# Kernel tuning notes

Measured on AMD Instinct MI355X. Metric: run time of the kernel, lower is better.

## Reference

```python
import jax, jax.numpy as jnp
import numpy as np

NEG_SLOPE = 0.2  # PyG GATConv default negative_slope
EPS = 1e-16      # PyG softmax denominator epsilon


def setup_inputs() -> dict:
    key = jax.random.key(0)
    N, C, H, E = 50000, 64, 12, 400000
    k = jax.random.split(key, 5)
    x = jax.random.normal(k[0], (N, C), dtype=jnp.float32)
    edge_index = jax.random.randint(k[1], (2, E), 0, N, dtype=jnp.int32)
    W = jax.random.normal(k[2], (C, H * C), dtype=jnp.float32) * (1.0 / np.sqrt(C))
    att_src = jax.random.normal(k[3], (H, C), dtype=jnp.float32) * 0.1
    att_dst = jax.random.normal(k[4], (H, C), dtype=jnp.float32) * 0.1
    bias = jnp.zeros((C,), dtype=jnp.float32)
    return {"x": x, "edge_index": edge_index, "W": W,
            "att_src": att_src, "att_dst": att_dst, "bias": bias}


def reference(x, edge_index, W, att_src, att_dst, bias):
    N, C = x.shape
    H = att_src.shape[0]
    # GATConv default add_self_loops=True
    loops = jnp.arange(N, dtype=edge_index.dtype)
    src = jnp.concatenate([edge_index[0], loops])  # message source j
    dst = jnp.concatenate([edge_index[1], loops])  # message target i

    h = (x @ W).reshape(N, H, C)                   # [N,H,C] projected features
    a_src = jnp.einsum('nhc,hc->nh', h, att_src)   # [N,H]
    a_dst = jnp.einsum('nhc,hc->nh', h, att_dst)   # [N,H]

    alpha = jax.nn.leaky_relu(a_src[src] + a_dst[dst], NEG_SLOPE)  # [E',H]
    # segment softmax over destination neighborhoods
    m = jax.ops.segment_max(alpha, dst, num_segments=N)
    alpha = jnp.exp(alpha - m[dst])
    denom = jax.ops.segment_sum(alpha, dst, num_segments=N)
    alpha = alpha / (denom[dst] + EPS)

    msg = h[src] * alpha[:, :, None]               # [E',H,C]
    out = jax.ops.segment_sum(msg, dst, num_segments=N)  # [N,H,C]
    y = out.mean(axis=1) + bias                    # concat=False -> head mean
    return jax.nn.relu(x + y)
```

## Files before the change

### kernel.cpp

```cpp
#include <hip/hip_runtime.h>
#include <hip/hip_bf16.h>


typedef __bf16 bf16x8 __attribute__((ext_vector_type(8)));
typedef float  f32x4  __attribute__((ext_vector_type(4)));
typedef float  f32x2  __attribute__((ext_vector_type(2)));

#define HEADS 12
#define CH 64
#define HC 768
#define CAP 64
#define ACOLS 24
#define ZSTRIDE 776

__device__ inline float readlane_f(float v, int lane) {
    return __builtin_bit_cast(float,
        __builtin_amdgcn_readlane(__builtin_bit_cast(int, v), lane));
}

__global__ __launch_bounds__(256) void k_pre(
    const float* __restrict__ W,
    const float* __restrict__ att_src, const float* __restrict__ att_dst,
    int* __restrict__ cnt, __bf16* __restrict__ Wt2, __bf16* __restrict__ Vt,
    int N) {
    const int nb_z = (N + 255) >> 8;
    const int nb_w = (CH * HC) >> 8;
    int b = blockIdx.x, tid = threadIdx.x;
    if (b < nb_z) {
        int i = b * 256 + tid;
        if (i < N) cnt[i] = 0;
        return;
    }
    b -= nb_z;
    if (b < nb_w) {
        int t = b * 256 + tid;
        int c = t / HC, kk = t % HC;
        int k = kk & 63;
        Wt2[t] = (__bf16)W[(size_t)k * HC + (kk - k) + c];
        return;
    }
    b -= nb_w;
    if (b >= 2 * HEADS) {
        if (tid < CH) Vt[b * CH + tid] = (__bf16)0.f;
        return;
    }
    const float* att = (b < HEADS) ? att_src + b * CH
                                   : att_dst + (b - HEADS) * CH;
    int k = tid >> 2, cq = tid & 3;
    const float* wr = W + (size_t)k * HC + (b % HEADS) * CH + cq * 16;
    float s = 0.f;
#pragma unroll
    for (int j = 0; j < 16; ++j) s += wr[j] * att[cq * 16 + j];
    s += __shfl_xor(s, 1, 64);
    s += __shfl_xor(s, 2, 64);
    if (cq == 0) Vt[b * CH + k] = (__bf16)s;
}

__global__ __launch_bounds__(256) void k_main(
    const float* __restrict__ x, const int* __restrict__ ei,
    const __bf16* __restrict__ Vt,
    int* __restrict__ cnt, int* __restrict__ adj,
    __bf16* __restrict__ xb, float* __restrict__ a_all, int N, int E) {
    const int EP = E + N;
    const int nb_build = (EP + 255) >> 8;
    int b = blockIdx.x, tid = threadIdx.x;

    if (b < nb_build) {
        int e = b * 256 + tid;
        if (e < EP) {
            int d, s;
            if (e < E) { d = ei[E + e]; s = ei[e]; }
            else       { d = e - E;     s = d; }
            int pos = atomicAdd(&cnt[d], 1);
            if (pos < CAP) adj[d * CAP + pos] = s;
        }
        return;
    }
    b -= nb_build;
    int wave = tid >> 6, lane = tid & 63;
    int m = lane & 15, quad = lane >> 4;
    int m0 = b * 64 + wave * 16;
    int row = m0 + m;
    int rc = row < N ? row : N - 1;
    const float* xa = x + (size_t)rc * CH + quad * 8;
    f32x4 v0 = *(const f32x4*)xa;
    f32x4 v1 = *(const f32x4*)(xa + 4);
    f32x4 v2 = *(const f32x4*)(xa + 32);
    f32x4 v3 = *(const f32x4*)(xa + 36);
    bf16x8 a0, a1;
#pragma unroll
    for (int j = 0; j < 4; ++j) {
        a0[j] = (__bf16)v0[j]; a0[4 + j] = (__bf16)v1[j];
        a1[j] = (__bf16)v2[j]; a1[4 + j] = (__bf16)v3[j];
    }
    if (row < N) {
        *(bf16x8*)(xb + (size_t)row * CH + quad * 8) = a0;
        *(bf16x8*)(xb + (size_t)row * CH + quad * 8 + 32) = a1;
    }
#pragma unroll
    for (int t = 0; t < 2; ++t) {
        const __bf16* bp = Vt + (size_t)(t * 16 + m) * CH + quad * 8;
        bf16x8 b0 = *(const bf16x8*)bp;
        bf16x8 b1 = *(const bf16x8*)(bp + 32);
        f32x4 acc = {0.f, 0.f, 0.f, 0.f};
        acc = __builtin_amdgcn_mfma_f32_16x16x32_bf16(a0, b0, acc, 0, 0, 0);
        acc = __builtin_amdgcn_mfma_f32_16x16x32_bf16(a1, b1, acc, 0, 0, 0);
        int col = t * 16 + m;
        if (col < ACOLS) {
#pragma unroll
            for (int r = 0; r < 4; ++r) {
                int rr = m0 + quad * 4 + r;
                if (rr < N) a_all[(size_t)rr * ACOLS + col] = acc[r];
            }
        }
    }
}

__global__ __launch_bounds__(256) void k_fused(
    const int* __restrict__ cnt, const int* __restrict__ adj,
    const float* __restrict__ a_all,
    const __bf16* __restrict__ xb, const __bf16* __restrict__ Wt2,
    const float* __restrict__ x, const float* __restrict__ bias,
    float* __restrict__ out, int N) {
    __shared__ __bf16 zt[16 * ZSTRIDE];
    int wave = threadIdx.x >> 6, lane = threadIdx.x & 63;
    int base = blockIdx.x * 16;

    int degj[4], slj[4];
#pragma unroll
    for (int j = 0; j < 4; ++j) {
        int d = base + wave * 4 + j;
        int dg = cnt[d];
        degj[j] = dg < CAP ? dg : CAP;
        int sraw = 0;
        if (lane < 32) sraw = adj[d * CAP + lane];
        slj[j] = sraw;
    }

    for (int j = 0; j < 4; ++j) {
        int row = wave * 4 + j;
        int d = base + row;
        int deg = degj[j];
        int s_l = slj[j];
        if (deg > 32 && lane >= 32)
            s_l = adj[d * CAP + lane];
        s_l = s_l < 0 ? 0 : (s_l >= N ? N - 1 : s_l);

        float adf[HEADS];
        {
            const f32x4* p = (const f32x4*)(a_all + (size_t)d * ACOLS + HEADS);
            f32x4 t0 = p[0], t1 = p[1], t2 = p[2];
#pragma unroll
            for (int u = 0; u < 4; ++u) { adf[u] = t0[u]; adf[4 + u] = t1[u]; adf[8 + u] = t2[u]; }
        }
        float w[HEADS];
        {
            const f32x4* p = (const f32x4*)(a_all + (size_t)s_l * ACOLS);
            f32x4 t0 = p[0], t1 = p[1], t2 = p[2];
            float asf[HEADS];
#pragma unroll
            for (int u = 0; u < 4; ++u) { asf[u] = t0[u]; asf[4 + u] = t1[u]; asf[8 + u] = t2[u]; }
#pragma unroll
            for (int hh = 0; hh < HEADS; ++hh) {
                float sc = asf[hh] + adf[hh];
                sc = sc > 0.f ? sc : 0.2f * sc;
                w[hh] = __expf(sc);
            }
        }

        f32x2 acc2[HEADS];
#pragma unroll
        for (int hh = 0; hh < HEADS; ++hh) acc2[hh] = (f32x2){0.f, 0.f};
        int i = 0;
        for (; i + 3 < deg; i += 4) {
            int s0 = __builtin_amdgcn_readlane(s_l, i);
            int s1 = __builtin_amdgcn_readlane(s_l, i + 1);
            int s2 = __builtin_amdgcn_readlane(s_l, i + 2);
            int s3 = __builtin_amdgcn_readlane(s_l, i + 3);
            f32x2 xv0 = {(float)xb[(size_t)s0 * CH + lane], 1.f};
            f32x2 xv1 = {(float)xb[(size_t)s1 * CH + lane], 1.f};
            f32x2 xv2 = {(float)xb[(size_t)s2 * CH + lane], 1.f};
            f32x2 xv3 = {(float)xb[(size_t)s3 * CH + lane], 1.f};
#pragma unroll
            for (int hh = 0; hh < HEADS; ++hh) {
                float w0 = readlane_f(w[hh], i);
                float w1 = readlane_f(w[hh], i + 1);
                float w2 = readlane_f(w[hh], i + 2);
                float w3 = readlane_f(w[hh], i + 3);
                acc2[hh] += (f32x2){w0, w0} * xv0;
                acc2[hh] += (f32x2){w1, w1} * xv1;
                acc2[hh] += (f32x2){w2, w2} * xv2;
                acc2[hh] += (f32x2){w3, w3} * xv3;
            }
        }
        for (; i < deg; ++i) {
            int s = __builtin_amdgcn_readlane(s_l, i);
            f32x2 xv = {(float)xb[(size_t)s * CH + lane], 1.f};
#pragma unroll
            for (int hh = 0; hh < HEADS; ++hh) {
                float wv = readlane_f(w[hh], i);
                acc2[hh] += (f32x2){wv, wv} * xv;
            }
        }
        __bf16* zr = zt + row * ZSTRIDE + lane;
#pragma unroll
        for (int hh = 0; hh < HEADS; ++hh)
            zr[hh * CH] = (__bf16)(acc2[hh].x * (1.0f / ((acc2[hh].y + 1e-16f) * HEADS)));
    }

    __syncthreads();

    {
        int m = lane & 15, quad = lane >> 4;
        int n0 = wave * 16;
        const __bf16* za = zt + m * ZSTRIDE + quad * 8;
        const __bf16* wb = Wt2 + (size_t)(n0 + m) * HC + quad * 8;
        f32x4 acc = {0.f, 0.f, 0.f, 0.f};
#pragma unroll
        for (int kc = 0; kc < HC; kc += 32) {
            bf16x8 a  = *(const bf16x8*)(za + kc);
            bf16x8 bf = *(const bf16x8*)(wb + kc);
            acc = __builtin_amdgcn_mfma_f32_16x16x32_bf16(a, bf, acc, 0, 0, 0);
        }
        int col = n0 + m;
        float bv = bias[col];
#pragma unroll
        for (int r = 0; r < 4; ++r) {
            int dd = base + quad * 4 + r;
            if (dd < N) {
                float o = x[(size_t)dd * CH + col] + acc[r] + bv;
                out[(size_t)dd * CH + col] = fmaxf(o, 0.f);
            }
        }
    }
}

extern "C" void kernel_launch(void* const* d_in, const int* in_sizes, int n_in,
                              void* d_out, int out_size, void* d_ws, size_t ws_size,
                              hipStream_t stream) {
    const float* x       = (const float*)d_in[0];
    const int*   ei      = (const int*)d_in[1];
    const float* W       = (const float*)d_in[2];
    const float* att_src = (const float*)d_in[3];
    const float* att_dst = (const float*)d_in[4];
    const float* bias    = (const float*)d_in[5];
    float* out = (float*)d_out;

    int N = in_sizes[0] / CH;
    int E = in_sizes[1] / 2;
    int EP = E + N;

    char* ws = (char*)d_ws;
    size_t off = 0;
    auto take = [&](size_t bytes) -> void* {
        void* p = ws + off;
        off = (off + bytes + 255) & ~(size_t)255;
        return p;
    };
    __bf16* xb    = (__bf16*)take((size_t)N * CH * sizeof(__bf16));
    __bf16* Wt2   = (__bf16*)take((size_t)CH * HC * sizeof(__bf16));
    __bf16* Vt    = (__bf16*)take((size_t)32 * CH * sizeof(__bf16));
    float*  a_all = (float*)take((size_t)N * ACOLS * sizeof(float));
    int*    adj   = (int*)take((size_t)N * CAP * sizeof(int));
    int*    cnt   = (int*)take((size_t)N * sizeof(int));

    const int nb_z     = (N + 255) / 256;
    const int nb_w     = (CH * HC) / 256;
    const int nb_build = (EP + 255) / 256;
    const int nb_ax    = (N + 63) / 64;

    k_pre<<<nb_z + nb_w + 32, 256, 0, stream>>>(W, att_src, att_dst, cnt, Wt2, Vt, N);
    k_main<<<nb_build + nb_ax, 256, 0, stream>>>(x, ei, Vt, cnt, adj, xb, a_all, N, E);
    k_fused<<<(N + 15) / 16, 256, 0, stream>>>(cnt, adj, a_all, xb, Wt2, x, bias, out, N);
}
```

Measured before the change: 176.4 us.

## Compute per-head neighbor aggregation with MFMA over LDS-staged gathered features

Result: slower. 185.9 us (+5.4%).

```diff
diff --git a/kernel.cpp b/kernel.cpp
--- a/kernel.cpp
+++ b/kernel.cpp
@@ -4,7 +4,6 @@
 
 typedef __bf16 bf16x8 __attribute__((ext_vector_type(8)));
 typedef float  f32x4  __attribute__((ext_vector_type(4)));
-typedef float  f32x2  __attribute__((ext_vector_type(2)));
 
 #define HEADS 12
 #define CH 64
@@ -12,11 +11,7 @@
 #define CAP 64
 #define ACOLS 24
 #define ZSTRIDE 776
-
-__device__ inline float readlane_f(float v, int lane) {
-    return __builtin_bit_cast(float,
-        __builtin_amdgcn_readlane(__builtin_bit_cast(int, v), lane));
-}
+#define XSTR 40
 
 __global__ __launch_bounds__(256) void k_pre(
     const float* __restrict__ W,
@@ -123,8 +118,17 @@
     const float* __restrict__ x, const float* __restrict__ bias,
     float* __restrict__ out, int N) {
     __shared__ __bf16 zt[16 * ZSTRIDE];
+    __shared__ __bf16 Xg[4][CH * XSTR];
+    __shared__ __bf16 Wl[4][16 * XSTR];
     int wave = threadIdx.x >> 6, lane = threadIdx.x & 63;
     int base = blockIdx.x * 16;
+
+    {
+        int* p = (int*)Xg[wave];
+        for (int i = lane; i < CH * XSTR / 2; i += 64) p[i] = 0;
+        int* q = (int*)Wl[wave];
+        for (int i = lane; i < 16 * XSTR / 2; i += 64) q[i] = 0;
+    }
 
     int degj[4], slj[4];
 #pragma unroll
@@ -132,19 +136,20 @@
         int d = base + wave * 4 + j;
         int dg = cnt[d];
         degj[j] = dg < CAP ? dg : CAP;
-        int sraw = 0;
-        if (lane < 32) sraw = adj[d * CAP + lane];
-        slj[j] = sraw;
-    }
+        slj[j] = (lane < 32) ? adj[d * CAP + lane] : 0;
+    }
+
+    bf16x8 onesb;
+#pragma unroll
+    for (int j = 0; j < 8; ++j) onesb[j] = (__bf16)1.0f;
+
+    int m = lane & 15, quad = lane >> 4;
+    int slot = lane >> 1, half = lane & 1;
 
     for (int j = 0; j < 4; ++j) {
         int row = wave * 4 + j;
         int d = base + row;
         int deg = degj[j];
-        int s_l = slj[j];
-        if (deg > 32 && lane >= 32)
-            s_l = adj[d * CAP + lane];
-        s_l = s_l < 0 ? 0 : (s_l >= N ? N - 1 : s_l);
 
         float adf[HEADS];
         {
@@ -153,65 +158,82 @@
 #pragma unroll
             for (int u = 0; u < 4; ++u) { adf[u] = t0[u]; adf[4 + u] = t1[u]; adf[8 + u] = t2[u]; }
         }
-        float w[HEADS];
-        {
-            const f32x4* p = (const f32x4*)(a_all + (size_t)s_l * ACOLS);
-            f32x4 t0 = p[0], t1 = p[1], t2 = p[2];
-            float asf[HEADS];
-#pragma unroll
-            for (int u = 0; u < 4; ++u) { asf[u] = t0[u]; asf[4 + u] = t1[u]; asf[8 + u] = t2[u]; }
-#pragma unroll
-            for (int hh = 0; hh < HEADS; ++hh) {
-                float sc = asf[hh] + adf[hh];
-                sc = sc > 0.f ? sc : 0.2f * sc;
-                w[hh] = __expf(sc);
-            }
-        }
-
-        f32x2 acc2[HEADS];
-#pragma unroll
-        for (int hh = 0; hh < HEADS; ++hh) acc2[hh] = (f32x2){0.f, 0.f};
-        int i = 0;
-        for (; i + 3 < deg; i += 4) {
-            int s0 = __builtin_amdgcn_readlane(s_l, i);
-            int s1 = __builtin_amdgcn_readlane(s_l, i + 1);
-            int s2 = __builtin_amdgcn_readlane(s_l, i + 2);
-            int s3 = __builtin_amdgcn_readlane(s_l, i + 3);
-            f32x2 xv0 = {(float)xb[(size_t)s0 * CH + lane], 1.f};
-            f32x2 xv1 = {(float)xb[(size_t)s1 * CH + lane], 1.f};
-            f32x2 xv2 = {(float)xb[(size_t)s2 * CH + lane], 1.f};
-            f32x2 xv3 = {(float)xb[(size_t)s3 * CH + lane], 1.f};
-#pragma unroll
-            for (int hh = 0; hh < HEADS; ++hh) {
-                float w0 = readlane_f(w[hh], i);
-                float w1 = readlane_f(w[hh], i + 1);
-                float w2 = readlane_f(w[hh], i + 2);
-                float w3 = readlane_f(w[hh], i + 3);
-                acc2[hh] += (f32x2){w0, w0} * xv0;
-                acc2[hh] += (f32x2){w1, w1} * xv1;
-                acc2[hh] += (f32x2){w2, w2} * xv2;
-                acc2[hh] += (f32x2){w3, w3} * xv3;
-            }
-        }
-        for (; i < deg; ++i) {
-            int s = __builtin_amdgcn_readlane(s_l, i);
-            f32x2 xv = {(float)xb[(size_t)s * CH + lane], 1.f};
-#pragma unroll
-            for (int hh = 0; hh < HEADS; ++hh) {
-                float wv = readlane_f(w[hh], i);
-                acc2[hh] += (f32x2){wv, wv} * xv;
-            }
-        }
-        __bf16* zr = zt + row * ZSTRIDE + lane;
-#pragma unroll
-        for (int hh = 0; hh < HEADS; ++hh)
-            zr[hh * CH] = (__bf16)(acc2[hh].x * (1.0f / ((acc2[hh].y + 1e-16f) * HEADS)));
+
+        f32x4 acc[4], den;
+#pragma unroll
+        for (int t = 0; t < 4; ++t) acc[t] = (f32x4){0.f, 0.f, 0.f, 0.f};
+        den = (f32x4){0.f, 0.f, 0.f, 0.f};
+
+        int nkh = (deg > 32) ? 2 : 1;
+        for (int kh = 0; kh < nkh; ++kh) {
+            int sb = kh * 32;
+            int ch_cnt = deg - sb; ch_cnt = ch_cnt > 32 ? 32 : ch_cnt;
+
+            int s_w = (kh == 0) ? slj[j]
+                                : ((lane < 32) ? adj[d * CAP + 32 + lane] : 0);
+            float wv[HEADS];
+#pragma unroll
+            for (int hh = 0; hh < HEADS; ++hh) wv[hh] = 0.f;
+            if (lane < ch_cnt) {
+                const f32x4* p = (const f32x4*)(a_all + (size_t)s_w * ACOLS);
+                f32x4 t0 = p[0], t1 = p[1], t2 = p[2];
+                float asf[HEADS];
+#pragma unroll
+                for (int u = 0; u < 4; ++u) { asf[u] = t0[u]; asf[4 + u] = t1[u]; asf[8 + u] = t2[u]; }
+#pragma unroll
+                for (int hh = 0; hh < HEADS; ++hh) {
+                    float sc = asf[hh] + adf[hh];
+                    sc = sc > 0.f ? sc : 0.2f * sc;
+                    wv[hh] = __expf(sc);
+                }
+            }
+            if (lane < 32) {
+                __bf16* wrow = Wl[wave];
+#pragma unroll
+                for (int hh = 0; hh < HEADS; ++hh)
+                    wrow[hh * XSTR + lane] = (__bf16)wv[hh];
+            }
+
+            if (slot < ch_cnt) {
+                int ss = adj[d * CAP + sb + slot];
+                const bf16x8* src = (const bf16x8*)(xb + (size_t)ss * CH + half * 32);
+                bf16x8 v0 = src[0], v1 = src[1], v2 = src[2], v3 = src[3];
+                __bf16* xg = Xg[wave];
+                int chb = half * 32;
+#pragma unroll
+                for (int c = 0; c < 8; ++c) {
+                    xg[(chb + c) * XSTR + slot]      = v0[c];
+                    xg[(chb + 8 + c) * XSTR + slot]  = v1[c];
+                    xg[(chb + 16 + c) * XSTR + slot] = v2[c];
+                    xg[(chb + 24 + c) * XSTR + slot] = v3[c];
+                }
+            }
+
+            bf16x8 afrag = *(const bf16x8*)(Wl[wave] + m * XSTR + quad * 8);
+            den = __builtin_amdgcn_mfma_f32_16x16x32_bf16(afrag, onesb, den, 0, 0, 0);
+#pragma unroll
+            for (int t = 0; t < 4; ++t) {
+                bf16x8 bfrag = *(const bf16x8*)(Xg[wave] + (t * 16 + m) * XSTR + quad * 8);
+                acc[t] = __builtin_amdgcn_mfma_f32_16x16x32_bf16(afrag, bfrag, acc[t], 0, 0, 0);
+            }
+        }
+
+        if (quad < 3) {
+            __bf16* zr = zt + row * ZSTRIDE;
+#pragma unroll
+            for (int r = 0; r < 4; ++r) {
+                int head = quad * 4 + r;
+                float inv = 1.0f / ((den[r] + 1e-16f) * HEADS);
+#pragma unroll
+                for (int t = 0; t < 4; ++t)
+                    zr[head * CH + t * 16 + m] = (__bf16)(acc[t][r] * inv);
+            }
+        }
     }
 
     __syncthreads();
 
     {
-        int m = lane & 15, quad = lane >> 4;
         int n0 = wave * 16;
         const __bf16* za = zt + m * ZSTRIDE + quad * 8;
         const __bf16* wb = Wt2 + (size_t)(n0 + m) * HC + quad * 8;
```

## Fold preprocessing kernel into main kernel, recompute attention vectors per block in LDS

Applied to the files above, without the earlier changes.

After: 338.2 us. 91.7% more time.

```diff
diff --git a/kernel.cpp b/kernel.cpp
--- a/kernel.cpp
+++ b/kernel.cpp
@@ -12,57 +12,23 @@
 #define CAP 64
 #define ACOLS 24
 #define ZSTRIDE 776
+#define VTSTR 72
 
 __device__ inline float readlane_f(float v, int lane) {
     return __builtin_bit_cast(float,
         __builtin_amdgcn_readlane(__builtin_bit_cast(int, v), lane));
 }
 
-__global__ __launch_bounds__(256) void k_pre(
+__global__ __launch_bounds__(256) void k_main(
+    const float* __restrict__ x, const int* __restrict__ ei,
     const float* __restrict__ W,
     const float* __restrict__ att_src, const float* __restrict__ att_dst,
-    int* __restrict__ cnt, __bf16* __restrict__ Wt2, __bf16* __restrict__ Vt,
-    int N) {
-    const int nb_z = (N + 255) >> 8;
-    const int nb_w = (CH * HC) >> 8;
-    int b = blockIdx.x, tid = threadIdx.x;
-    if (b < nb_z) {
-        int i = b * 256 + tid;
-        if (i < N) cnt[i] = 0;
-        return;
-    }
-    b -= nb_z;
-    if (b < nb_w) {
-        int t = b * 256 + tid;
-        int c = t / HC, kk = t % HC;
-        int k = kk & 63;
-        Wt2[t] = (__bf16)W[(size_t)k * HC + (kk - k) + c];
-        return;
-    }
-    b -= nb_w;
-    if (b >= 2 * HEADS) {
-        if (tid < CH) Vt[b * CH + tid] = (__bf16)0.f;
-        return;
-    }
-    const float* att = (b < HEADS) ? att_src + b * CH
-                                   : att_dst + (b - HEADS) * CH;
-    int k = tid >> 2, cq = tid & 3;
-    const float* wr = W + (size_t)k * HC + (b % HEADS) * CH + cq * 16;
-    float s = 0.f;
-#pragma unroll
-    for (int j = 0; j < 16; ++j) s += wr[j] * att[cq * 16 + j];
-    s += __shfl_xor(s, 1, 64);
-    s += __shfl_xor(s, 2, 64);
-    if (cq == 0) Vt[b * CH + k] = (__bf16)s;
-}
-
-__global__ __launch_bounds__(256) void k_main(
-    const float* __restrict__ x, const int* __restrict__ ei,
-    const __bf16* __restrict__ Vt,
     int* __restrict__ cnt, int* __restrict__ adj,
-    __bf16* __restrict__ xb, float* __restrict__ a_all, int N, int E) {
+    __bf16* __restrict__ xb, __bf16* __restrict__ Wt2,
+    float* __restrict__ a_all, int N, int E) {
     const int EP = E + N;
     const int nb_build = (EP + 255) >> 8;
+    const int nb_w     = (CH * HC) >> 8;
     int b = blockIdx.x, tid = threadIdx.x;
 
     if (b < nb_build) {
@@ -77,40 +43,77 @@
         return;
     }
     b -= nb_build;
+    if (b < nb_w) {
+        int t = b * 256 + tid;
+        int c = t / HC, kk = t % HC;
+        int k = kk & 63;
+        Wt2[t] = (__bf16)W[(size_t)k * HC + (kk - k) + c];
+        return;
+    }
+    b -= nb_w;
+    __shared__ __bf16 VtL[32 * VTSTR];
     int wave = tid >> 6, lane = tid & 63;
+
+    for (int i = tid; i < 32 * VTSTR; i += 256) VtL[i] = (__bf16)0.f;
+    __syncthreads();
+
+#pragma unroll
+    for (int cidx = 0; cidx < 6; ++cidx) {
+        int col = wave * 6 + cidx;
+        const float* att = (col < HEADS) ? att_src + col * CH
+                                         : att_dst + (col - HEADS) * CH;
+        float av = att[lane];
+        int hb = (col % HEADS) * CH;
+#pragma unroll 4
+        for (int k = 0; k < CH; ++k) {
+            float p = W[(size_t)k * HC + hb + lane] * av;
+            p += __shfl_xor(p, 1, 64);
+            p += __shfl_xor(p, 2, 64);
+            p += __shfl_xor(p, 4, 64);
+            p += __shfl_xor(p, 8, 64);
+            p += __shfl_xor(p, 16, 64);
+            p += __shfl_xor(p, 32, 64);
+            if (lane == 0) VtL[col * VTSTR + k] = (__bf16)p;
+        }
+    }
+    __syncthreads();
+
     int m = lane & 15, quad = lane >> 4;
-    int m0 = b * 64 + wave * 16;
-    int row = m0 + m;
-    int rc = row < N ? row : N - 1;
-    const float* xa = x + (size_t)rc * CH + quad * 8;
-    f32x4 v0 = *(const f32x4*)xa;
-    f32x4 v1 = *(const f32x4*)(xa + 4);
-    f32x4 v2 = *(const f32x4*)(xa + 32);
-    f32x4 v3 = *(const f32x4*)(xa + 36);
-    bf16x8 a0, a1;
-#pragma unroll
-    for (int j = 0; j < 4; ++j) {
-        a0[j] = (__bf16)v0[j]; a0[4 + j] = (__bf16)v1[j];
-        a1[j] = (__bf16)v2[j]; a1[4 + j] = (__bf16)v3[j];
-    }
-    if (row < N) {
-        *(bf16x8*)(xb + (size_t)row * CH + quad * 8) = a0;
-        *(bf16x8*)(xb + (size_t)row * CH + quad * 8 + 32) = a1;
-    }
-#pragma unroll
-    for (int t = 0; t < 2; ++t) {
-        const __bf16* bp = Vt + (size_t)(t * 16 + m) * CH + quad * 8;
-        bf16x8 b0 = *(const bf16x8*)bp;
-        bf16x8 b1 = *(const bf16x8*)(bp + 32);
-        f32x4 acc = {0.f, 0.f, 0.f, 0.f};
-        acc = __builtin_amdgcn_mfma_f32_16x16x32_bf16(a0, b0, acc, 0, 0, 0);
-        acc = __builtin_amdgcn_mfma_f32_16x16x32_bf16(a1, b1, acc, 0, 0, 0);
-        int col = t * 16 + m;
-        if (col < ACOLS) {
-#pragma unroll
-            for (int r = 0; r < 4; ++r) {
-                int rr = m0 + quad * 4 + r;
-                if (rr < N) a_all[(size_t)rr * ACOLS + col] = acc[r];
+#pragma unroll
+    for (int t16 = 0; t16 < 4; ++t16) {
+        int m0 = b * 256 + (t16 * 4 + wave) * 16;
+        int row = m0 + m;
+        int rc = row < N ? row : N - 1;
+        const float* xa = x + (size_t)rc * CH + quad * 8;
+        f32x4 v0 = *(const f32x4*)xa;
+        f32x4 v1 = *(const f32x4*)(xa + 4);
+        f32x4 v2 = *(const f32x4*)(xa + 32);
+        f32x4 v3 = *(const f32x4*)(xa + 36);
+        bf16x8 a0, a1;
+#pragma unroll
+        for (int j = 0; j < 4; ++j) {
+            a0[j] = (__bf16)v0[j]; a0[4 + j] = (__bf16)v1[j];
+            a1[j] = (__bf16)v2[j]; a1[4 + j] = (__bf16)v3[j];
+        }
+        if (row < N) {
+            *(bf16x8*)(xb + (size_t)row * CH + quad * 8) = a0;
+            *(bf16x8*)(xb + (size_t)row * CH + quad * 8 + 32) = a1;
+        }
+#pragma unroll
+        for (int t = 0; t < 2; ++t) {
+            const __bf16* bp = VtL + (size_t)(t * 16 + m) * VTSTR + quad * 8;
+            bf16x8 b0 = *(const bf16x8*)bp;
+            bf16x8 b1 = *(const bf16x8*)(bp + 32);
+            f32x4 acc = {0.f, 0.f, 0.f, 0.f};
+            acc = __builtin_amdgcn_mfma_f32_16x16x32_bf16(a0, b0, acc, 0, 0, 0);
+            acc = __builtin_amdgcn_mfma_f32_16x16x32_bf16(a1, b1, acc, 0, 0, 0);
+            int col = t * 16 + m;
+            if (col < ACOLS) {
+#pragma unroll
+                for (int r = 0; r < 4; ++r) {
+                    int rr = m0 + quad * 4 + r;
+                    if (rr < N) a_all[(size_t)rr * ACOLS + col] = acc[r];
+                }
             }
         }
     }
@@ -132,9 +135,7 @@
         int d = base + wave * 4 + j;
         int dg = cnt[d];
         degj[j] = dg < CAP ? dg : CAP;
-        int sraw = 0;
-        if (lane < 32) sraw = adj[d * CAP + lane];
-        slj[j] = sraw;
+        slj[j] = (lane < 32) ? adj[d * CAP + lane] : 0;
     }
 
     for (int j = 0; j < 4; ++j) {
@@ -259,17 +260,18 @@
     };
     __bf16* xb    = (__bf16*)take((size_t)N * CH * sizeof(__bf16));
     __bf16* Wt2   = (__bf16*)take((size_t)CH * HC * sizeof(__bf16));
-    __bf16* Vt    = (__bf16*)take((size_t)32 * CH * sizeof(__bf16));
     float*  a_all = (float*)take((size_t)N * ACOLS * sizeof(float));
     int*    adj   = (int*)take((size_t)N * CAP * sizeof(int));
     int*    cnt   = (int*)take((size_t)N * sizeof(int));
 
-    const int nb_z     = (N + 255) / 256;
+    hipMemsetAsync(cnt, 0, (size_t)N * sizeof(int), stream);
+
+    const int nb_build = (EP + 255) / 256;
     const int nb_w     = (CH * HC) / 256;
-    const int nb_build = (EP + 255) / 256;
-    const int nb_ax    = (N + 63) / 64;
-
-    k_pre<<<nb_z + nb_w + 32, 256, 0, stream>>>(W, att_src, att_dst, cnt, Wt2, Vt, N);
-    k_main<<<nb_build + nb_ax, 256, 0, stream>>>(x, ei, Vt, cnt, adj, xb, a_all, N, E);
-    k_fused<<<(N + 15) / 16, 256, 0, stream>>>(cnt, adj, a_all, xb, Wt2, x, bias, out, N);
-}
+    const int nb_ax    = (N + 255) / 256;
+
+    k_main<<<nb_build + nb_w + nb_ax, 256, 0, stream>>>(
+        x, ei, W, att_src, att_dst, cnt, adj, xb, Wt2, a_all, N, E);
+    k_fused<<<(N + 15) / 16, 256, 0, stream>>>(
+        cnt, adj, a_all, xb, Wt2, x, bias, out, N);
+}
```

## Prefetch attention scores for next row and pad degree loop to multiples of four

Applied to the files above, without the earlier changes.

New measurement: 179.9 us. +2.0%, slower.

```diff
diff --git a/kernel.cpp b/kernel.cpp
--- a/kernel.cpp
+++ b/kernel.cpp
@@ -132,47 +132,58 @@
         int d = base + wave * 4 + j;
         int dg = cnt[d];
         degj[j] = dg < CAP ? dg : CAP;
-        int sraw = 0;
-        if (lane < 32) sraw = adj[d * CAP + lane];
-        slj[j] = sraw;
-    }
-
-    for (int j = 0; j < 4; ++j) {
+        int sraw = (lane < 32) ? adj[d * CAP + lane] : 0;
+        slj[j] = sraw < 0 ? 0 : (sraw >= N ? N - 1 : sraw);
+    }
+#pragma unroll
+    for (int j = 0; j < 4; ++j) {
+        if (degj[j] > 32 && lane >= 32) {
+            int sraw = adj[(base + wave * 4 + j) * CAP + lane];
+            slj[j] = sraw < 0 ? 0 : (sraw >= N ? N - 1 : sraw);
+        }
+    }
+
+    f32x4 asb[2][3], adb[2][3];
+    {
+        const f32x4* pa = (const f32x4*)(a_all + (size_t)(base + wave * 4) * ACOLS + HEADS);
+        adb[0][0] = pa[0]; adb[0][1] = pa[1]; adb[0][2] = pa[2];
+        const f32x4* ps = (const f32x4*)(a_all + (size_t)slj[0] * ACOLS);
+        asb[0][0] = ps[0]; asb[0][1] = ps[1]; asb[0][2] = ps[2];
+    }
+
+#pragma unroll
+    for (int j = 0; j < 4; ++j) {
+        int cur = j & 1, nxt = cur ^ 1;
         int row = wave * 4 + j;
-        int d = base + row;
         int deg = degj[j];
+        int deg4 = (deg + 3) & ~3;
         int s_l = slj[j];
-        if (deg > 32 && lane >= 32)
-            s_l = adj[d * CAP + lane];
-        s_l = s_l < 0 ? 0 : (s_l >= N ? N - 1 : s_l);
-
-        float adf[HEADS];
-        {
-            const f32x4* p = (const f32x4*)(a_all + (size_t)d * ACOLS + HEADS);
-            f32x4 t0 = p[0], t1 = p[1], t2 = p[2];
-#pragma unroll
-            for (int u = 0; u < 4; ++u) { adf[u] = t0[u]; adf[4 + u] = t1[u]; adf[8 + u] = t2[u]; }
-        }
+
         float w[HEADS];
         {
-            const f32x4* p = (const f32x4*)(a_all + (size_t)s_l * ACOLS);
-            f32x4 t0 = p[0], t1 = p[1], t2 = p[2];
-            float asf[HEADS];
-#pragma unroll
-            for (int u = 0; u < 4; ++u) { asf[u] = t0[u]; asf[4 + u] = t1[u]; asf[8 + u] = t2[u]; }
-#pragma unroll
-            for (int hh = 0; hh < HEADS; ++hh) {
-                float sc = asf[hh] + adf[hh];
-                sc = sc > 0.f ? sc : 0.2f * sc;
-                w[hh] = __expf(sc);
-            }
+            float pad = (lane < deg) ? 0.f : -1e30f;
+#pragma unroll
+            for (int g = 0; g < 3; ++g) {
+#pragma unroll
+                for (int u = 0; u < 4; ++u) {
+                    float sc = asb[cur][g][u] + adb[cur][g][u];
+                    sc = sc > 0.f ? sc : 0.2f * sc;
+                    w[g * 4 + u] = __expf(sc + pad);
+                }
+            }
+        }
+
+        if (j < 3) {
+            const f32x4* pa = (const f32x4*)(a_all + (size_t)(base + wave * 4 + j + 1) * ACOLS + HEADS);
+            adb[nxt][0] = pa[0]; adb[nxt][1] = pa[1]; adb[nxt][2] = pa[2];
+            const f32x4* ps = (const f32x4*)(a_all + (size_t)slj[j + 1] * ACOLS);
+            asb[nxt][0] = ps[0]; asb[nxt][1] = ps[1]; asb[nxt][2] = ps[2];
         }
 
         f32x2 acc2[HEADS];
 #pragma unroll
         for (int hh = 0; hh < HEADS; ++hh) acc2[hh] = (f32x2){0.f, 0.f};
-        int i = 0;
-        for (; i + 3 < deg; i += 4) {
+        for (int i = 0; i < deg4; i += 4) {
             int s0 = __builtin_amdgcn_readlane(s_l, i);
             int s1 = __builtin_amdgcn_readlane(s_l, i + 1);
             int s2 = __builtin_amdgcn_readlane(s_l, i + 2);
@@ -191,15 +202,6 @@
                 acc2[hh] += (f32x2){w1, w1} * xv1;
                 acc2[hh] += (f32x2){w2, w2} * xv2;
                 acc2[hh] += (f32x2){w3, w3} * xv3;
-            }
-        }
-        for (; i < deg; ++i) {
-            int s = __builtin_amdgcn_readlane(s_l, i);
-            f32x2 xv = {(float)xb[(size_t)s * CH + lane], 1.f};
-#pragma unroll
-            for (int hh = 0; hh < HEADS; ++hh) {
-                float wv = readlane_f(w[hh], i);
-                acc2[hh] += (f32x2){wv, wv} * xv;
             }
         }
         __bf16* zr = zt + row * ZSTRIDE + lane;
```
